# Optimization experiments

Hardware: AMD Instinct MI355X
Metric: run time of the kernel (lower is better)

Reference implementation:

```python
import jax, jax.numpy as jnp
import numpy as np

EPS = 1e-10
REG = 1e-6  # regularization_weight passed to sparse_image_warp


def _phi(r2):
    # order-2 polyharmonic (thin-plate) kernel: 0.5 * r^2 * log(r^2)
    return 0.5 * r2 * jnp.log(jnp.maximum(r2, EPS))


def _tps_interpolate(train_pts, train_vals, query_pts, reg):
    # train_pts: (B,N,2), train_vals: (B,N,2), query_pts: (B,Q,2)
    b, n, _ = train_pts.shape
    d2 = jnp.sum((train_pts[:, :, None, :] - train_pts[:, None, :, :]) ** 2, -1)
    A = _phi(d2) + reg * jnp.eye(n, dtype=train_pts.dtype)  # (B,N,N)
    ones_n = jnp.ones((b, n, 1), train_pts.dtype)
    Bm = jnp.concatenate([train_pts, ones_n], -1)  # (B,N,3)
    top = jnp.concatenate([A, Bm], -1)
    bot = jnp.concatenate([jnp.swapaxes(Bm, 1, 2), jnp.zeros((b, 3, 3), train_pts.dtype)], -1)
    lhs = jnp.concatenate([top, bot], 1)  # (B,N+3,N+3)
    rhs = jnp.concatenate([train_vals, jnp.zeros((b, 3, train_vals.shape[-1]), train_vals.dtype)], 1)
    sol = jnp.linalg.solve(lhs, rhs)
    w, v = sol[:, :n], sol[:, n:]  # rbf weights (B,N,2), affine (B,3,2)
    q2 = jnp.sum((query_pts[:, :, None, :] - train_pts[:, None, :, :]) ** 2, -1)  # (B,Q,N)
    rbf = jnp.einsum('bqn,bnd->bqd', _phi(q2), w)
    ones_q = jnp.ones((b, query_pts.shape[1], 1), query_pts.dtype)
    lin = jnp.einsum('bqk,bkd->bqd', jnp.concatenate([query_pts, ones_q], -1), v)
    return rbf + lin


def _bilinear_sample(image, qy, qx):
    # image: (B,H,W,C); qy,qx: (B,Q) float query coordinates (TF dense_image_warp clamping)
    B, H, W, C = image.shape
    y0 = jnp.clip(jnp.floor(qy), 0, H - 2).astype(jnp.int32)
    x0 = jnp.clip(jnp.floor(qx), 0, W - 2).astype(jnp.int32)
    ay = jnp.clip(qy - y0.astype(qy.dtype), 0.0, 1.0)[..., None]
    ax = jnp.clip(qx - x0.astype(qx.dtype), 0.0, 1.0)[..., None]
    bi = jnp.arange(B)[:, None]
    g = lambda yi, xi: image[bi, yi, xi]  # gather -> (B,Q,C)
    top = g(y0, x0) * (1 - ax) + g(y0, x0 + 1) * ax
    bot = g(y0 + 1, x0) * (1 - ax) + g(y0 + 1, x0 + 1) * ax
    return top * (1 - ay) + bot * ay


def _sparse_image_warp(image, src, dst, reg):
    # TF semantics: flows at control points = dst - src, interpolated at dst; sample at grid - flow
    B, H, W, C = image.shape
    flows_ctrl = dst - src  # (B,N,2)
    gy, gx = jnp.meshgrid(jnp.arange(H, dtype=image.dtype), jnp.arange(W, dtype=image.dtype), indexing='ij')
    grid = jnp.broadcast_to(jnp.stack([gy, gx], -1).reshape(1, H * W, 2), (B, H * W, 2))
    dense_flow = _tps_interpolate(dst, flows_ctrl, grid, reg)  # (B,HW,2)
    query = grid - dense_flow
    warped = _bilinear_sample(image, query[..., 0], query[..., 1])
    return warped.reshape(B, H, W, C), dense_flow.reshape(B, H, W, 2)


def setup_inputs() -> dict:
    key = jax.random.key(0)
    ks = jax.random.split(key, 8)
    B, C, H, W = 16, 64, 112, 112
    n_ldmark = 16
    F = C * H * W
    x = jax.random.normal(ks[0], (B, C, H, W), jnp.float32)
    images_rendered = jax.random.normal(ks[1], (B, H, W, C), jnp.float32)
    scales = jax.random.uniform(ks[2], (B, 1), jnp.float32)
    W1 = jax.random.normal(ks[3], (128, F), jnp.float32) / np.float32(np.sqrt(F))
    b1 = jnp.zeros((128,), jnp.float32)
    W2 = jax.random.normal(ks[4], (n_ldmark * 2, 128), jnp.float32) / np.float32(np.sqrt(128))
    b2 = jnp.zeros((n_ldmark * 2,), jnp.float32)
    W3 = jax.random.normal(ks[5], (n_ldmark * 2, 128), jnp.float32) / np.float32(np.sqrt(128))
    b3 = jnp.zeros((n_ldmark * 2,), jnp.float32)
    # torch.normal(mean=0, std=50, size=(n_ldmark,2)) + [0.5*H, 0.5*W], fixed for determinism
    landmarks_mean = jax.random.normal(ks[6], (n_ldmark, 2), jnp.float32) * 50.0 \
        + jnp.array([0.5 * H, 0.5 * W], jnp.float32)
    return {"x": x, "images_rendered": images_rendered, "scales": scales,
            "W1": W1, "b1": b1, "W2": W2, "b2": b2, "W3": W3, "b3": b3,
            "landmarks_mean": landmarks_mean}


def reference(x, images_rendered, scales, W1, b1, W2, b2, W3, b3, landmarks_mean):
    B = x.shape[0]
    n_ldmark = landmarks_mean.shape[0]
    feat = x.reshape(B, -1)
    out = feat @ W1.T + b1  # (B,128)
    landmarks_pred = out @ W2.T + b2 + landmarks_mean.reshape(-1)  # (B, 2*n_ldmark)
    landmarks_disp = (out @ W3.T + b3) * scales
    # original uses .detach().clone() on landmark coords -> stop_gradient
    src = jax.lax.stop_gradient(landmarks_pred).reshape(B, n_ldmark, 2)
    dst = jax.lax.stop_gradient(landmarks_pred + landmarks_disp).reshape(B, n_ldmark, 2)
    # torch.norm(..., dim=(1,2)) = per-batch Frobenius norm, then mean
    landmarks_norm = jnp.mean(jnp.sqrt(jnp.sum((src - dst) ** 2, axis=(1, 2))))
    warped, _dense_flow = _sparse_image_warp(images_rendered, src, dst, REG)
    images_transformed = jnp.transpose(warped, (0, 3, 1, 2))  # NHWC -> NCHW
    return images_transformed, landmarks_pred, landmarks_norm
```

## Files before the change

### kernel.cpp

```cpp
#include <hip/hip_runtime.h>
#include <math.h>
#include <stdint.h>

#define F_K 802816
#define KC 1024
#define NB1 784
#define PRED_OFF 12845056
#define NORM_OFF 12845568

#define AS3 __attribute__((address_space(3)))
#define AS1 __attribute__((address_space(1)))

__device__ __forceinline__ void gload16(const float* gsrc, float* ldsbase) {
  __builtin_amdgcn_global_load_lds((const AS1 uint32_t*)gsrc, (AS3 uint32_t*)ldsbase, 16, 0, 0);
}

__global__ __launch_bounds__(256) void k_gemm1(const float* __restrict__ x,
                                               const float* __restrict__ w1,
                                               float* __restrict__ part) {
  __shared__ __align__(16) float xs[256 * 4];
  __shared__ __align__(16) float ws[2048 * 4];
  const int t = threadIdx.x;
  const int wave = t >> 6, lane = t & 63;
  const int nl = t & 15;
  const int bg = (t >> 4) & 3;
  const size_t k0 = (size_t)blockIdx.x * KC;

  const float* wsrc[8];
#pragma unroll
  for (int cc = 0; cc < 8; ++cc) {
    int flat = cc * 64 + lane;
    int n = flat >> 2, tau = flat & 3;
    int q = (tau - (n >> 1)) & 3;
    wsrc[cc] = w1 + (size_t)n * F_K + k0 + 16 * wave + 4 * q;
  }
  const float* xsrc;
  {
    int b = lane >> 2, tau = lane & 3;
    int q = (tau - (b >> 1)) & 3;
    xsrc = x + (size_t)b * F_K + k0 + 16 * wave + 4 * q;
  }
  float* xbase = xs + wave * 256;
  float* wbase = ws + wave * 2048;

  float acc[4][8];
#pragma unroll
  for (int i = 0; i < 4; ++i)
#pragma unroll
    for (int j = 0; j < 8; ++j) acc[i][j] = 0.f;

  for (int kt = 0; kt < KC / 64; ++kt) {
    asm volatile("s_waitcnt lgkmcnt(0)" ::: "memory");
    gload16(xsrc + kt * 64, xbase);
#pragma unroll
    for (int cc = 0; cc < 8; ++cc) gload16(wsrc[cc] + kt * 64, wbase + cc * 256);
    asm volatile("s_waitcnt vmcnt(0)" ::: "memory");
    __builtin_amdgcn_sched_barrier(0);
#pragma unroll
    for (int q = 0; q < 4; ++q) {
      float4 xv[4];
#pragma unroll
      for (int i = 0; i < 4; ++i) {
        int b = 4 * bg + i;
        int tx = (q + (b >> 1)) & 3;
        xv[i] = *reinterpret_cast<const float4*>(&xbase[b * 16 + 4 * tx]);
      }
      const int tw = (q + (nl >> 1)) & 3;
#pragma unroll
      for (int j = 0; j < 8; ++j) {
        float4 wv = *reinterpret_cast<const float4*>(&wbase[(16 * j + nl) * 16 + 4 * tw]);
#pragma unroll
        for (int i = 0; i < 4; ++i) {
          acc[i][j] += xv[i].x * wv.x;
          acc[i][j] += xv[i].y * wv.y;
          acc[i][j] += xv[i].z * wv.z;
          acc[i][j] += xv[i].w * wv.w;
        }
      }
    }
  }

  __syncthreads();
  float* red = ws;
#pragma unroll
  for (int i = 0; i < 4; ++i)
#pragma unroll
    for (int j = 0; j < 8; ++j)
      red[wave * 2048 + (4 * bg + i) * 128 + 16 * j + nl] = acc[i][j];
  __syncthreads();
  const int o8 = t * 8;
  float4 s0 = {0, 0, 0, 0}, s1 = {0, 0, 0, 0};
#pragma unroll
  for (int w = 0; w < 4; ++w) {
    float4 a = *reinterpret_cast<const float4*>(&red[w * 2048 + o8]);
    float4 b = *reinterpret_cast<const float4*>(&red[w * 2048 + o8 + 4]);
    s0.x += a.x; s0.y += a.y; s0.z += a.z; s0.w += a.w;
    s1.x += b.x; s1.y += b.y; s1.z += b.z; s1.w += b.w;
  }
  float* pp = part + (size_t)blockIdx.x * 2048 + o8;
  *reinterpret_cast<float4*>(pp) = s0;
  *reinterpret_cast<float4*>(pp + 4) = s1;
}

__global__ __launch_bounds__(256) void k_red(const float* __restrict__ part,
                                             float* __restrict__ p2) {
  int pc = blockIdx.x >> 3, ib = blockIdx.x & 7;
  int idx = ib * 256 + threadIdx.x;
  const float* p = part + (size_t)pc * 49 * 2048 + idx;
  float s = 0.f;
  for (int q = 0; q < 49; ++q) s += p[(size_t)q * 2048];
  p2[pc * 2048 + idx] = s;
}

__global__ __launch_bounds__(64) void k_small(const float* __restrict__ p2,
    const float* __restrict__ b1, const float* __restrict__ W2, const float* __restrict__ b2,
    const float* __restrict__ W3, const float* __restrict__ b3,
    const float* __restrict__ lmean, const float* __restrict__ scales,
    float* __restrict__ dout_pred, float* __restrict__ coef, float* __restrict__ norms) {
  const int b = blockIdx.x, lane = threadIdx.x;
  __shared__ float o[128], dflat[32], fl[32], A[19][22], farr[19], sol[19][2];

  for (int h = 0; h < 2; ++h) {
    int n = lane + 64 * h;
    float s = b1[n];
    for (int pc = 0; pc < 16; ++pc) s += p2[pc * 2048 + b * 128 + n];
    o[n] = s;
  }
  __syncthreads();

  const int j = lane & 31;
  const float* Wm = (lane < 32) ? (W2 + j * 128) : (W3 + j * 128);
  float acc = 0.f;
#pragma unroll 4
  for (int n = 0; n < 128; ++n) acc += o[n] * Wm[n];
  float other = __shfl(acc, j + 32);
  float sc = scales[b];
  float dspv = 0.f;
  if (lane < 32) {
    float predv = acc + b2[j] + lmean[j];
    dspv = (other + b3[j]) * sc;
    dout_pred[b * 32 + j] = predv;
    dflat[j] = predv + dspv;
    fl[j] = dspv;
  }
  float s2 = (lane < 32) ? dspv * dspv : 0.f;
  for (int off = 32; off; off >>= 1) s2 += __shfl_xor(s2, off);
  if (lane == 0) norms[b] = sqrtf(s2);
  __syncthreads();

  for (int cell = lane; cell < 19 * 21; cell += 64) {
    int r = cell / 21, c = cell - (cell / 21) * 21;
    float v;
    if (r < 16) {
      if (c < 16) {
        float dy = dflat[2*r] - dflat[2*c], dx = dflat[2*r+1] - dflat[2*c+1];
        float d2 = dy * dy + dx * dx;
        v = 0.5f * d2 * logf(fmaxf(d2, 1e-10f));
        if (r == c) v += 1e-6f;
      } else if (c == 16) v = dflat[2*r];
      else if (c == 17) v = dflat[2*r+1];
      else if (c == 18) v = 1.0f;
      else if (c == 19) v = fl[2*r];
      else               v = fl[2*r+1];
    } else {
      int rr = r - 16;
      if (c < 16) v = (rr == 0) ? dflat[2*c] : (rr == 1) ? dflat[2*c+1] : 1.0f;
      else        v = 0.0f;
    }
    A[r][c] = v;
  }
  __syncthreads();

  for (int k = 0; k < 19; ++k) {
    float av = (lane >= k && lane < 19) ? fabsf(A[lane][k]) : -1.0f;
    int idx = lane;
    for (int off = 32; off; off >>= 1) {
      float v2 = __shfl_xor(av, off);
      int  i2 = __shfl_xor(idx, off);
      if (v2 > av) { av = v2; idx = i2; }
    }
    idx = __shfl(idx, 0);
    if (idx != k && lane < 21) {
      float tmp = A[k][lane]; A[k][lane] = A[idx][lane]; A[idx][lane] = tmp;
    }
    __syncthreads();
    float invp = 1.0f / A[k][k];
    if (lane < 19) farr[lane] = (lane > k) ? A[lane][k] * invp : 0.0f;
    __syncthreads();
    int nr = 18 - k, nc = 20 - k;
    for (int cell = lane; cell < nr * nc; cell += 64) {
      int i = k + 1 + cell / nc, jj = k + 1 + cell % nc;
      A[i][jj] -= farr[i] * A[k][jj];
    }
    __syncthreads();
  }
  for (int k = 18; k >= 0; --k) {
    if (lane < 2) sol[k][lane] = A[k][19 + lane] / A[k][k];
    __syncthreads();
    if (lane < 2 * k) {
      int i = lane >> 1, c = lane & 1;
      A[i][19 + c] -= A[i][k] * sol[k][c];
    }
    __syncthreads();
  }
  float* cf = coef + b * 80;
  if (lane < 32) { cf[lane] = sol[lane >> 1][lane & 1]; cf[38 + lane] = dflat[lane]; }
  else if (lane < 38) cf[lane] = sol[16 + ((lane - 32) >> 1)][(lane - 32) & 1];
}

__global__ __launch_bounds__(256) void k_warp(const float* __restrict__ img,
                                              const float* __restrict__ coef,
                                              const float* __restrict__ norms,
                                              float* __restrict__ out) {
  const int bid = blockIdx.x;
  const int b = bid / 112, y = bid - (bid / 112) * 112;
  const int t = threadIdx.x;
  __shared__ float qy[112], qx[112];
  __shared__ float cw[32], cv[6], cd[32];
  __shared__ float tile[64][113];

  if (bid == 0 && t == 0) {
    float s = 0.f;
    for (int i = 0; i < 16; ++i) s += norms[i];
    out[NORM_OFF] = s * (1.0f / 16.0f);
  }
  const float* cf = coef + b * 80;
  if (t < 70) {
    float v = cf[t];
    if (t < 32) cw[t] = v;
    else if (t < 38) cv[t - 32] = v;
    else cd[t - 38] = v;
  }
  __syncthreads();

  if (t < 112) {
    float fy = (float)y, fx = (float)t;
    float s0 = cv[0] * fy + cv[2] * fx + cv[4];
    float s1 = cv[1] * fy + cv[3] * fx + cv[5];
#pragma unroll
    for (int i = 0; i < 16; ++i) {
      float dy = fy - cd[2 * i], dx = fx - cd[2 * i + 1];
      float d2 = dy * dy + dx * dx;
      float ph = 0.5f * d2 * logf(fmaxf(d2, 1e-10f));
      s0 += ph * cw[2 * i];
      s1 += ph * cw[2 * i + 1];
    }
    qy[t] = fy - s0;
    qx[t] = fx - s1;
  }
  __syncthreads();

  const int wave = t >> 6, lane = t & 63;
#pragma unroll 4
  for (int p = 0; p < 28; ++p) {
    int xx = wave * 28 + p;
    float fy = qy[xx], fx = qx[xx];
    float y0f = fminf(fmaxf(floorf(fy), 0.f), 110.f);
    float x0f = fminf(fmaxf(floorf(fx), 0.f), 110.f);
    float ay = fminf(fmaxf(fy - y0f, 0.f), 1.f);
    float ax = fminf(fmaxf(fx - x0f, 0.f), 1.f);
    int y0 = (int)y0f, x0 = (int)x0f;
    const float* p00 = img + (((size_t)(b * 112 + y0) * 112 + x0) * 64) + lane;
    float v00 = p00[0], v01 = p00[64];
    float v10 = p00[112 * 64], v11 = p00[112 * 64 + 64];
    float top = v00 * (1.f - ax) + v01 * ax;
    float bot = v10 * (1.f - ax) + v11 * ax;
    tile[lane][xx] = top * (1.f - ay) + bot * ay;
  }
  __syncthreads();

  float* ob = out + (size_t)b * 64 * 12544 + y * 112;
  for (int i = 0; i < 28; ++i) {
    int idx = i * 256 + t;
    int c = idx / 112, xx = idx - c * 112;
    ob[(size_t)c * 12544 + xx] = tile[c][xx];
  }
}

extern "C" void kernel_launch(void* const* d_in, const int* in_sizes, int n_in,
                              void* d_out, int out_size, void* d_ws, size_t ws_size,
                              hipStream_t stream) {
  const float* x      = (const float*)d_in[0];
  const float* img    = (const float*)d_in[1];
  const float* scales = (const float*)d_in[2];
  const float* W1     = (const float*)d_in[3];
  const float* b1     = (const float*)d_in[4];
  const float* W2     = (const float*)d_in[5];
  const float* b2     = (const float*)d_in[6];
  const float* W3     = (const float*)d_in[7];
  const float* b3     = (const float*)d_in[8];
  const float* lmean  = (const float*)d_in[9];
  float* out = (float*)d_out;
  float* ws  = (float*)d_ws;

  float* P1   = ws;
  float* P2   = P1 + (size_t)NB1 * 2048;
  float* COEF = P2 + 16 * 2048;
  float* NORM = COEF + 16 * 80;

  k_gemm1<<<NB1, 256, 0, stream>>>(x, W1, P1);
  k_red  <<<128, 256, 0, stream>>>(P1, P2);
  k_small<<<16, 64, 0, stream>>>(P2, b1, W2, b2, W3, b3, lmean, scales,
                                 out + PRED_OFF, COEF, NORM);
  k_warp <<<16 * 112, 256, 0, stream>>>(img, COEF, NORM, out);
}
```

Before: 177.7 us.

## Double-buffer LDS tiles in gemm1 to overlap global loads with compute

The gemm1 K-loop now uses two LDS buffers and prefetches the tile two iterations ahead with global_load_lds. It waits only on the older batch (vmcnt(9)), so the next tile's loads are in flight while the current tile is computed. This targets load-latency stalls in a GEMV-like, bandwidth-bound loop, at the cost of doubling the LDS footprint, which may lower occupancy.

```diff
diff --git a/kernel.cpp b/kernel.cpp
--- a/kernel.cpp
+++ b/kernel.cpp
@@ -18,8 +18,8 @@
 __global__ __launch_bounds__(256) void k_gemm1(const float* __restrict__ x,
                                                const float* __restrict__ w1,
                                                float* __restrict__ part) {
-  __shared__ __align__(16) float xs[256 * 4];
-  __shared__ __align__(16) float ws[2048 * 4];
+  __shared__ __align__(16) float xs[2][256 * 4];
+  __shared__ __align__(16) float ws[2][2048 * 4];
   const int t = threadIdx.x;
   const int wave = t >> 6, lane = t & 63;
   const int nl = t & 15;
@@ -40,8 +40,8 @@
     int q = (tau - (b >> 1)) & 3;
     xsrc = x + (size_t)b * F_K + k0 + 16 * wave + 4 * q;
   }
-  float* xbase = xs + wave * 256;
-  float* wbase = ws + wave * 2048;
+  float* xbase[2] = { &xs[0][wave * 256], &xs[1][wave * 256] };
+  float* wbase[2] = { &ws[0][wave * 2048], &ws[1][wave * 2048] };
 
   float acc[4][8];
 #pragma unroll
@@ -49,13 +49,25 @@
 #pragma unroll
     for (int j = 0; j < 8; ++j) acc[i][j] = 0.f;
 
+#pragma unroll
+  for (int pt = 0; pt < 2; ++pt) {
+    gload16(xsrc + pt * 64, xbase[pt]);
+#pragma unroll
+    for (int cc = 0; cc < 8; ++cc) gload16(wsrc[cc] + pt * 64, wbase[pt] + cc * 256);
+  }
+  __builtin_amdgcn_sched_barrier(0);
+
+#pragma unroll 2
   for (int kt = 0; kt < KC / 64; ++kt) {
-    asm volatile("s_waitcnt lgkmcnt(0)" ::: "memory");
-    gload16(xsrc + kt * 64, xbase);
-#pragma unroll
-    for (int cc = 0; cc < 8; ++cc) gload16(wsrc[cc] + kt * 64, wbase + cc * 256);
-    asm volatile("s_waitcnt vmcnt(0)" ::: "memory");
+    const int cur = kt & 1;
+    if (kt < KC / 64 - 1) {
+      asm volatile("s_waitcnt vmcnt(9)" ::: "memory");
+    } else {
+      asm volatile("s_waitcnt vmcnt(0)" ::: "memory");
+    }
     __builtin_amdgcn_sched_barrier(0);
+    const float* xb = xbase[cur];
+    const float* wb = wbase[cur];
 #pragma unroll
     for (int q = 0; q < 4; ++q) {
       float4 xv[4];
@@ -63,12 +75,12 @@
       for (int i = 0; i < 4; ++i) {
         int b = 4 * bg + i;
         int tx = (q + (b >> 1)) & 3;
-        xv[i] = *reinterpret_cast<const float4*>(&xbase[b * 16 + 4 * tx]);
+        xv[i] = *reinterpret_cast<const float4*>(&xb[b * 16 + 4 * tx]);
       }
       const int tw = (q + (nl >> 1)) & 3;
 #pragma unroll
       for (int j = 0; j < 8; ++j) {
-        float4 wv = *reinterpret_cast<const float4*>(&wbase[(16 * j + nl) * 16 + 4 * tw]);
+        float4 wv = *reinterpret_cast<const float4*>(&wb[(16 * j + nl) * 16 + 4 * tw]);
 #pragma unroll
         for (int i = 0; i < 4; ++i) {
           acc[i][j] += xv[i].x * wv.x;
@@ -78,10 +90,19 @@
         }
       }
     }
-  }
-
-  __syncthreads();
-  float* red = ws;
+    __builtin_amdgcn_sched_barrier(0);
+    asm volatile("s_waitcnt lgkmcnt(0)" ::: "memory");
+    if (kt + 2 < KC / 64) {
+      gload16(xsrc + (kt + 2) * 64, xbase[cur]);
+#pragma unroll
+      for (int cc = 0; cc < 8; ++cc)
+        gload16(wsrc[cc] + (kt + 2) * 64, wbase[cur] + cc * 256);
+    }
+    __builtin_amdgcn_sched_barrier(0);
+  }
+
+  __syncthreads();
+  float* red = &ws[0][0];
 #pragma unroll
   for (int i = 0; i < 4; ++i)
 #pragma unroll
```

Result: slower. 211.1 us (+18.8%).

## Restructure GEMM1 split-K with preloaded x window and staggered W loads

Applied to the files above, without the earlier changes.

The first GEMM is split into twice as many K windows of 512, with blocks requesting two waves per SIMD through launch bounds. Each block preloads its whole x window into padded LDS once, then streams W1 tiles whose k-order is rotated per row group so different rows hit different addresses. The partial-sum reduction becomes a single pass of 8 blocks over 1568 partials, and k_small no longer sums 16 second-level partials. This aims to raise memory-level parallelism and occupancy on the bandwidth-bound W1 stream, at the cost of a longer serial reduction with very few blocks.

```diff
diff --git a/kernel.cpp b/kernel.cpp
--- a/kernel.cpp
+++ b/kernel.cpp
@@ -3,8 +3,9 @@
 #include <stdint.h>
 
 #define F_K 802816
-#define KC 1024
-#define NB1 784
+#define NWIN 1568
+#define WIN 512
+#define NT 8
 #define PRED_OFF 12845056
 #define NORM_OFF 12845568
 
@@ -14,34 +15,39 @@
 __device__ __forceinline__ void gload16(const float* gsrc, float* ldsbase) {
   __builtin_amdgcn_global_load_lds((const AS1 uint32_t*)gsrc, (AS3 uint32_t*)ldsbase, 16, 0, 0);
 }
-
-__global__ __launch_bounds__(256) void k_gemm1(const float* __restrict__ x,
-                                               const float* __restrict__ w1,
-                                               float* __restrict__ part) {
-  __shared__ __align__(16) float xs[256 * 4];
-  __shared__ __align__(16) float ws[2048 * 4];
+__device__ __forceinline__ void gload4(const float* gsrc, float* ldsbase) {
+  __builtin_amdgcn_global_load_lds((const AS1 uint32_t*)gsrc, (AS3 uint32_t*)ldsbase, 4, 0, 0);
+}
+
+__global__ __launch_bounds__(256, 2) void k_gemm1(const float* __restrict__ x,
+                                                  const float* __restrict__ w1,
+                                                  float* __restrict__ part) {
+  __shared__ __align__(16) float XL[8736];
+  __shared__ __align__(16) float WS[4 * 2048];
   const int t = threadIdx.x;
   const int wave = t >> 6, lane = t & 63;
   const int nl = t & 15;
   const int bg = (t >> 4) & 3;
-  const size_t k0 = (size_t)blockIdx.x * KC;
-
-  const float* wsrc[8];
+  const int c = blockIdx.x;
+  const size_t base = (size_t)c * WIN;
+
+  for (int s = 0; s < 32; ++s) {
+    int m = wave * 32 + s;
+    int T = m >> 4, b = m & 15;
+    gload4(x + (size_t)b * F_K + base + T * 64 + lane, XL + T * 1092 + b * 68);
+  }
+
+  const float* wsrcb[8];
+  int ph[8];
 #pragma unroll
   for (int cc = 0; cc < 8; ++cc) {
-    int flat = cc * 64 + lane;
-    int n = flat >> 2, tau = flat & 3;
-    int q = (tau - (n >> 1)) & 3;
-    wsrc[cc] = w1 + (size_t)n * F_K + k0 + 16 * wave + 4 * q;
-  }
-  const float* xsrc;
-  {
-    int b = lane >> 2, tau = lane & 3;
-    int q = (tau - (b >> 1)) & 3;
-    xsrc = x + (size_t)b * F_K + k0 + 16 * wave + 4 * q;
-  }
-  float* xbase = xs + wave * 256;
-  float* wbase = ws + wave * 2048;
+    int f = cc * 64 + lane;
+    int n = f >> 2, tau = f & 3;
+    int qr = (tau - (n >> 1)) & 3;
+    wsrcb[cc] = w1 + (size_t)n * F_K + base + 16 * wave + 4 * qr;
+    ph[cc] = n & 7;
+  }
+  float* wb = WS + wave * 2048;
 
   float acc[4][8];
 #pragma unroll
@@ -49,26 +55,29 @@
 #pragma unroll
     for (int j = 0; j < 8; ++j) acc[i][j] = 0.f;
 
-  for (int kt = 0; kt < KC / 64; ++kt) {
-    asm volatile("s_waitcnt lgkmcnt(0)" ::: "memory");
-    gload16(xsrc + kt * 64, xbase);
-#pragma unroll
-    for (int cc = 0; cc < 8; ++cc) gload16(wsrc[cc] + kt * 64, wbase + cc * 256);
+  asm volatile("s_waitcnt vmcnt(0)" ::: "memory");
+  __syncthreads();
+
+  const int Tl = nl & 7;
+  for (int kt = 0; kt < NT; ++kt) {
+#pragma unroll
+    for (int cc = 0; cc < 8; ++cc)
+      gload16(wsrcb[cc] + (((kt + ph[cc]) & 7) << 6), wb + cc * 256);
     asm volatile("s_waitcnt vmcnt(0)" ::: "memory");
     __builtin_amdgcn_sched_barrier(0);
+
+    const int Tx = (kt + Tl) & 7;
+    const int xo = Tx * 1092 + 16 * wave;
 #pragma unroll
     for (int q = 0; q < 4; ++q) {
       float4 xv[4];
 #pragma unroll
-      for (int i = 0; i < 4; ++i) {
-        int b = 4 * bg + i;
-        int tx = (q + (b >> 1)) & 3;
-        xv[i] = *reinterpret_cast<const float4*>(&xbase[b * 16 + 4 * tx]);
-      }
+      for (int i = 0; i < 4; ++i)
+        xv[i] = *reinterpret_cast<const float4*>(&XL[xo + (4 * bg + i) * 68 + 4 * q]);
       const int tw = (q + (nl >> 1)) & 3;
 #pragma unroll
       for (int j = 0; j < 8; ++j) {
-        float4 wv = *reinterpret_cast<const float4*>(&wbase[(16 * j + nl) * 16 + 4 * tw]);
+        float4 wv = *reinterpret_cast<const float4*>(&wb[(16 * j + nl) * 16 + 4 * tw]);
 #pragma unroll
         for (int i = 0; i < 4; ++i) {
           acc[i][j] += xv[i].x * wv.x;
@@ -78,10 +87,13 @@
         }
       }
     }
-  }
-
-  __syncthreads();
-  float* red = ws;
+    __builtin_amdgcn_sched_barrier(0);
+    asm volatile("s_waitcnt lgkmcnt(0)" ::: "memory");
+    __builtin_amdgcn_sched_barrier(0);
+  }
+
+  __syncthreads();
+  float* red = WS;
 #pragma unroll
   for (int i = 0; i < 4; ++i)
 #pragma unroll
@@ -97,19 +109,19 @@
     s0.x += a.x; s0.y += a.y; s0.z += a.z; s0.w += a.w;
     s1.x += b.x; s1.y += b.y; s1.z += b.z; s1.w += b.w;
   }
-  float* pp = part + (size_t)blockIdx.x * 2048 + o8;
+  float* pp = part + (size_t)c * 2048 + o8;
   *reinterpret_cast<float4*>(pp) = s0;
   *reinterpret_cast<float4*>(pp + 4) = s1;
 }
 
 __global__ __launch_bounds__(256) void k_red(const float* __restrict__ part,
                                              float* __restrict__ p2) {
-  int pc = blockIdx.x >> 3, ib = blockIdx.x & 7;
-  int idx = ib * 256 + threadIdx.x;
-  const float* p = part + (size_t)pc * 49 * 2048 + idx;
+  int idx = blockIdx.x * 256 + threadIdx.x;
+  const float* p = part + idx;
   float s = 0.f;
-  for (int q = 0; q < 49; ++q) s += p[(size_t)q * 2048];
-  p2[pc * 2048 + idx] = s;
+#pragma unroll 8
+  for (int q = 0; q < NWIN; ++q) s += p[(size_t)q * 2048];
+  p2[idx] = s;
 }
 
 __global__ __launch_bounds__(64) void k_small(const float* __restrict__ p2,
@@ -120,12 +132,8 @@
   const int b = blockIdx.x, lane = threadIdx.x;
   __shared__ float o[128], dflat[32], fl[32], A[19][22], farr[19], sol[19][2];
 
-  for (int h = 0; h < 2; ++h) {
-    int n = lane + 64 * h;
-    float s = b1[n];
-    for (int pc = 0; pc < 16; ++pc) s += p2[pc * 2048 + b * 128 + n];
-    o[n] = s;
-  }
+  o[lane]      = p2[b * 128 + lane]      + b1[lane];
+  o[lane + 64] = p2[b * 128 + 64 + lane] + b1[64 + lane];
   __syncthreads();
 
   const int j = lane & 31;
@@ -149,25 +157,25 @@
   __syncthreads();
 
   for (int cell = lane; cell < 19 * 21; cell += 64) {
-    int r = cell / 21, c = cell - (cell / 21) * 21;
+    int r = cell / 21, cc = cell - (cell / 21) * 21;
     float v;
     if (r < 16) {
-      if (c < 16) {
-        float dy = dflat[2*r] - dflat[2*c], dx = dflat[2*r+1] - dflat[2*c+1];
+      if (cc < 16) {
+        float dy = dflat[2*r] - dflat[2*cc], dx = dflat[2*r+1] - dflat[2*cc+1];
         float d2 = dy * dy + dx * dx;
         v = 0.5f * d2 * logf(fmaxf(d2, 1e-10f));
-        if (r == c) v += 1e-6f;
-      } else if (c == 16) v = dflat[2*r];
-      else if (c == 17) v = dflat[2*r+1];
-      else if (c == 18) v = 1.0f;
-      else if (c == 19) v = fl[2*r];
+        if (r == cc) v += 1e-6f;
+      } else if (cc == 16) v = dflat[2*r];
+      else if (cc == 17) v = dflat[2*r+1];
+      else if (cc == 18) v = 1.0f;
+      else if (cc == 19) v = fl[2*r];
       else               v = fl[2*r+1];
     } else {
       int rr = r - 16;
-      if (c < 16) v = (rr == 0) ? dflat[2*c] : (rr == 1) ? dflat[2*c+1] : 1.0f;
-      else        v = 0.0f;
-    }
-    A[r][c] = v;
+      if (cc < 16) v = (rr == 0) ? dflat[2*cc] : (rr == 1) ? dflat[2*cc+1] : 1.0f;
+      else         v = 0.0f;
+    }
+    A[r][cc] = v;
   }
   __syncthreads();
 
@@ -198,8 +206,8 @@
     if (lane < 2) sol[k][lane] = A[k][19 + lane] / A[k][k];
     __syncthreads();
     if (lane < 2 * k) {
-      int i = lane >> 1, c = lane & 1;
-      A[i][19 + c] -= A[i][k] * sol[k][c];
+      int i = lane >> 1, cc = lane & 1;
+      A[i][19 + cc] -= A[i][k] * sol[k][cc];
     }
     __syncthreads();
   }
@@ -272,8 +280,8 @@
   float* ob = out + (size_t)b * 64 * 12544 + y * 112;
   for (int i = 0; i < 28; ++i) {
     int idx = i * 256 + t;
-    int c = idx / 112, xx = idx - c * 112;
-    ob[(size_t)c * 12544 + xx] = tile[c][xx];
+    int cc = idx / 112, xx = idx - cc * 112;
+    ob[(size_t)cc * 12544 + xx] = tile[cc][xx];
   }
 }
 
@@ -294,12 +302,12 @@
   float* ws  = (float*)d_ws;
 
   float* P1   = ws;
-  float* P2   = P1 + (size_t)NB1 * 2048;
-  float* COEF = P2 + 16 * 2048;
+  float* P2   = P1 + (size_t)NWIN * 2048;
+  float* COEF = P2 + 2048;
   float* NORM = COEF + 16 * 80;
 
-  k_gemm1<<<NB1, 256, 0, stream>>>(x, W1, P1);
-  k_red  <<<128, 256, 0, stream>>>(P1, P2);
+  k_gemm1<<<NWIN, 256, 0, stream>>>(x, W1, P1);
+  k_red  <<<8, 256, 0, stream>>>(P1, P2);
   k_small<<<16, 64, 0, stream>>>(P2, b1, W2, b2, W3, b3, lmean, scales,
                                  out + PRED_OFF, COEF, NORM);
   k_warp <<<16 * 112, 256, 0, stream>>>(img, COEF, NORM, out);
```

Result: slower. 243.6 us (+37.1%).
